# Kernel tuning notes

Measured on AMD Instinct MI355X. Metric: run time of the kernel, lower is better.

## Reference

```python
import jax, jax.numpy as jnp
import numpy as np

N_QUBITS = 13
N_LAYERS = 8
DIM = 2 ** N_QUBITS
CDT = jnp.complex64

_X = jnp.array([[0.0, 1.0], [1.0, 0.0]], dtype=CDT)
_Z = jnp.array([[1.0, 0.0], [0.0, -1.0]], dtype=CDT)
_I2 = jnp.eye(2, dtype=CDT)
_CNOT = jnp.array([[1, 0, 0, 0], [0, 1, 0, 0], [0, 0, 0, 1], [0, 0, 1, 0]], dtype=CDT)


def build_ops():
    """Hardware-efficient ansatz: per layer RX on all qubits, RZ on all qubits, CNOT chain."""
    ops = []
    p = 0
    for _ in range(N_LAYERS):
        for q in range(N_QUBITS):
            ops.append(('RX', (q,), p)); p += 1
        for q in range(N_QUBITS):
            ops.append(('RZ', (q,), p)); p += 1
        for q in range(N_QUBITS - 1):
            ops.append(('CNOT', (q, q + 1), None))
    return ops, p

OPS, N_PARAMS = build_ops()


def _rot(generator, theta):
    # U = cos(theta/2) I - i sin(theta/2) G
    h = theta * 0.5
    return jnp.cos(h).astype(CDT) * _I2 - 1j * jnp.sin(h).astype(CDT) * generator


def _apply_1q(state, U, q):
    st = state.reshape((2,) * N_QUBITS)
    st = jnp.tensordot(U, st, axes=([1], [q]))  # contracted axis moves to front
    return jnp.moveaxis(st, 0, q).reshape(-1)


def _apply_2q(state, U, q0, q1):
    st = state.reshape((2,) * N_QUBITS)
    st = jnp.tensordot(U.reshape(2, 2, 2, 2), st, axes=([2, 3], [q0, q1]))
    return jnp.moveaxis(st, (0, 1), (q0, q1)).reshape(-1)


def _run_circuit(params):
    state = jnp.zeros(DIM, dtype=CDT).at[0].set(1.0)
    for gate, qubits, pidx in OPS:
        if gate == 'RX':
            state = _apply_1q(state, _rot(_X, params[pidx]), qubits[0])
        elif gate == 'RZ':
            state = _apply_1q(state, _rot(_Z, params[pidx]), qubits[0])
        else:  # CNOT
            state = _apply_2q(state, _CNOT, qubits[0], qubits[1])
    return state


def setup_inputs() -> dict:
    key = jax.random.key(0)
    k1, k2 = jax.random.split(key)
    params = jax.random.normal(k1, (N_PARAMS,), dtype=jnp.float32)
    observable = jax.random.normal(k2, (DIM, DIM), dtype=jnp.float32)
    return {"params": params, "observable": observable}


def reference(params, observable) -> jnp.ndarray:
    psi = _run_circuit(params)                      # [2^n] complex64
    obs_psi = observable.astype(CDT) @ psi          # dense observable matvec
    loss = jnp.vdot(psi, obs_psi).real.astype(jnp.float32)  # <psi|O|psi>
    return loss
```

## Files before the change

kernel.cpp:

```cpp
#include <hip/hip_runtime.h>

#define DIM 8192
#define NLAYERS 8
#define SIMT 512
#define QFB 2048
#define QFT 256
#define ROWS_PER_BLOCK 4

typedef float floatx4 __attribute__((ext_vector_type(4)));
typedef float f2 __attribute__((ext_vector_type(2)));

__device__ __forceinline__ int swz(int i) { return i ^ ((i >> 4) & 15); }

__global__ __launch_bounds__(SIMT) void sim_kernel(const float* __restrict__ params,
                                                   float* __restrict__ outR,
                                                   float* __restrict__ outM) {
    __shared__ f2 buf[2][DIM];
    const int t = threadIdx.x;

    f2 a[16];
#pragma unroll
    for (int l = 0; l < 16; ++l) a[l] = (f2){0.f, 0.f};
    if (t == 0) a[0] = (f2){1.f, 0.f};

    int pp = 0;

    for (int layer = 0; layer < NLAYERS; ++layer) {
        const float* __restrict__ prx = params + layer * 26;
        const float* __restrict__ prz = prx + 13;

        float cb[13], sb[13];
#pragma unroll
        for (int p = 0; p < 13; ++p) __sincosf(0.5f * prx[12 - p], &sb[p], &cb[p]);

#pragma unroll
        for (int k = 0; k < 4; ++k) {
            const f2 c2 = {cb[k], cb[k]};
            const f2 sg = {sb[k], -sb[k]};
#pragma unroll
            for (int l0 = 0; l0 < 16; ++l0) {
                if (!(l0 & (1 << k))) {
                    const int l1 = l0 | (1 << k);
                    const f2 a0 = a[l0], a1 = a[l1];
                    a[l0] = c2 * a0 + __builtin_shufflevector(a1, a1, 1, 0) * sg;
                    a[l1] = c2 * a1 + __builtin_shufflevector(a0, a0, 1, 0) * sg;
                }
            }
        }

        {
            f2* __restrict__ B = buf[pp]; pp ^= 1;
#pragma unroll
            for (int l = 0; l < 16; ++l) B[swz((t << 4) | l)] = a[l];
            __syncthreads();
#pragma unroll
            for (int l = 0; l < 16; ++l) a[l] = B[swz((t & 15) | (l << 4) | ((t >> 4) << 8))];
        }

#pragma unroll
        for (int k = 0; k < 4; ++k) {
            const f2 c2 = {cb[4 + k], cb[4 + k]};
            const f2 sg = {sb[4 + k], -sb[4 + k]};
#pragma unroll
            for (int l0 = 0; l0 < 16; ++l0) {
                if (!(l0 & (1 << k))) {
                    const int l1 = l0 | (1 << k);
                    const f2 a0 = a[l0], a1 = a[l1];
                    a[l0] = c2 * a0 + __builtin_shufflevector(a1, a1, 1, 0) * sg;
                    a[l1] = c2 * a1 + __builtin_shufflevector(a0, a0, 1, 0) * sg;
                }
            }
        }

        {
            f2* __restrict__ B = buf[pp]; pp ^= 1;
#pragma unroll
            for (int l = 0; l < 16; ++l) B[swz((t & 15) | (l << 4) | ((t >> 4) << 8))] = a[l];
            __syncthreads();
#pragma unroll
            for (int l = 0; l < 16; ++l)
                a[l] = B[swz(((t >> 1) & 255) | (l << 8) | ((t & 1) << 12))];
        }

#pragma unroll
        for (int k = 0; k < 4; ++k) {
            const f2 c2 = {cb[8 + k], cb[8 + k]};
            const f2 sg = {sb[8 + k], -sb[8 + k]};
#pragma unroll
            for (int l0 = 0; l0 < 16; ++l0) {
                if (!(l0 & (1 << k))) {
                    const int l1 = l0 | (1 << k);
                    const f2 a0 = a[l0], a1 = a[l1];
                    a[l0] = c2 * a0 + __builtin_shufflevector(a1, a1, 1, 0) * sg;
                    a[l1] = c2 * a1 + __builtin_shufflevector(a0, a0, 1, 0) * sg;
                }
            }
        }

        {
            const f2 c2 = {cb[12], cb[12]};
            const f2 sg = {sb[12], -sb[12]};
#pragma unroll
            for (int l = 0; l < 16; ++l) {
                f2 o;
                o.x = __shfl_xor(a[l].x, 1);
                o.y = __shfl_xor(a[l].y, 1);
                a[l] = c2 * a[l] + __builtin_shufflevector(o, o, 1, 0) * sg;
            }
        }

        float hz[13];
#pragma unroll
        for (int p = 0; p < 13; ++p) hz[p] = 0.5f * prz[12 - p];
        float phiT = 0.f;
#pragma unroll
        for (int p = 0; p < 8; ++p) phiT += (((t >> 1) >> p) & 1) ? hz[p] : -hz[p];
        phiT += (t & 1) ? hz[12] : -hz[12];
#pragma unroll
        for (int l = 0; l < 16; ++l) {
            float phi = phiT;
            phi += (l & 1) ? hz[8]  : -hz[8];
            phi += (l & 2) ? hz[9]  : -hz[9];
            phi += (l & 4) ? hz[10] : -hz[10];
            phi += (l & 8) ? hz[11] : -hz[11];
            float sp, cp;
            __sincosf(phi, &sp, &cp);
            a[l] = (f2){a[l].x * cp - a[l].y * sp, a[l].x * sp + a[l].y * cp};
        }

        {
            f2* __restrict__ B = buf[pp]; pp ^= 1;
#pragma unroll
            for (int l = 0; l < 16; ++l)
                B[swz(((t >> 1) & 255) | (l << 8) | ((t & 1) << 12))] = a[l];
            __syncthreads();
#pragma unroll
            for (int l = 0; l < 16; ++l) {
                const int c0 = (t << 4) | l;
                a[l] = B[swz(c0 ^ (c0 >> 1))];
            }
        }
    }

#pragma unroll
    for (int g = 0; g < 4; ++g) {
        const float4 rv = make_float4(a[4*g].x, a[4*g+1].x, a[4*g+2].x, a[4*g+3].x);
        const float4 mv = make_float4(a[4*g].y, a[4*g+1].y, a[4*g+2].y, a[4*g+3].y);
        ((float4*)outR)[(t << 2) + g] = rv;
        ((float4*)outM)[(t << 2) + g] = mv;
    }
}

__global__ __launch_bounds__(QFT) void quad_kernel(const float* __restrict__ O,
                                                   const float* __restrict__ R,
                                                   const float* __restrict__ M,
                                                   float* __restrict__ partials) {
    const int bi = blockIdx.x;
    const int t  = threadIdx.x;
    const float4* __restrict__ R4 = (const float4*)R;
    const float4* __restrict__ M4 = (const float4*)M;

    float acc = 0.f;
#pragma unroll
    for (int rr = 0; rr < ROWS_PER_BLOCK; ++rr) {
        const int i = bi * ROWS_PER_BLOCK + rr;
        const float ri = R[i];
        const float mi = M[i];
        const floatx4* __restrict__ Or = (const floatx4*)(O + (size_t)i * DIM);
#pragma unroll
        for (int it = 0; it < DIM / 4 / QFT; ++it) {
            const int j4 = t + it * QFT;
            const floatx4 o = __builtin_nontemporal_load(&Or[j4]);
            const float4 rj = R4[j4];
            const float4 mj = M4[j4];
            acc = fmaf(o.x, fmaf(ri, rj.x, mi * mj.x), acc);
            acc = fmaf(o.y, fmaf(ri, rj.y, mi * mj.y), acc);
            acc = fmaf(o.z, fmaf(ri, rj.z, mi * mj.z), acc);
            acc = fmaf(o.w, fmaf(ri, rj.w, mi * mj.w), acc);
        }
    }

#pragma unroll
    for (int off = 32; off > 0; off >>= 1) acc += __shfl_down(acc, off);
    __shared__ float wsum[QFT / 64];
    const int lane = t & 63, w = t >> 6;
    if (lane == 0) wsum[w] = acc;
    __syncthreads();
    if (t == 0) {
        float s = 0.f;
#pragma unroll
        for (int k = 0; k < QFT / 64; ++k) s += wsum[k];
        partials[bi] = s;
    }
}

__global__ __launch_bounds__(256) void reduce_kernel(const float* __restrict__ partials,
                                                     float* __restrict__ out) {
    const int t = threadIdx.x;
    float acc = 0.f;
#pragma unroll
    for (int k = 0; k < QFB / 256; ++k) acc += partials[t + k * 256];
#pragma unroll
    for (int off = 32; off > 0; off >>= 1) acc += __shfl_down(acc, off);
    __shared__ float wsum[4];
    const int lane = t & 63, w = t >> 6;
    if (lane == 0) wsum[w] = acc;
    __syncthreads();
    if (t == 0) out[0] = wsum[0] + wsum[1] + wsum[2] + wsum[3];
}

extern "C" void kernel_launch(void* const* d_in, const int* in_sizes, int n_in,
                              void* d_out, int out_size, void* d_ws, size_t ws_size,
                              hipStream_t stream) {
    const float* params = (const float*)d_in[0];
    const float* O      = (const float*)d_in[1];
    float* out = (float*)d_out;

    float* R        = (float*)d_ws;
    float* M        = R + DIM;
    float* partials = M + DIM;

    sim_kernel<<<1, SIMT, 0, stream>>>(params, R, M);
    quad_kernel<<<QFB, QFT, 0, stream>>>(O, R, M, partials);
    reduce_kernel<<<1, 256, 0, stream>>>(partials, out);
}
```

Baseline: 82.15 us.

## Double simulation threads to 1024 with 8 amplitudes each and four-stage exchange

The single-block statevector simulation now uses 1024 threads, each holding 8 amplitudes instead of 16. The qubit passes are regrouped into 3-qubit register stages, which adds one more shared-memory transpose and __syncthreads per layer. The aim is to shorten the serial per-thread dependency chain in the latency-bound single-block kernel, at the cost of more barriers and LDS traffic per layer.

```diff
diff --git a/kernel.cpp b/kernel.cpp
--- a/kernel.cpp
+++ b/kernel.cpp
@@ -2,7 +2,7 @@
 
 #define DIM 8192
 #define NLAYERS 8
-#define SIMT 512
+#define SIMT 1024
 #define QFB 2048
 #define QFT 256
 #define ROWS_PER_BLOCK 4
@@ -18,9 +18,9 @@
     __shared__ f2 buf[2][DIM];
     const int t = threadIdx.x;
 
-    f2 a[16];
-#pragma unroll
-    for (int l = 0; l < 16; ++l) a[l] = (f2){0.f, 0.f};
+    f2 a[8];
+#pragma unroll
+    for (int l = 0; l < 8; ++l) a[l] = (f2){0.f, 0.f};
     if (t == 0) a[0] = (f2){1.f, 0.f};
 
     int pp = 0;
@@ -34,60 +34,88 @@
         for (int p = 0; p < 13; ++p) __sincosf(0.5f * prx[12 - p], &sb[p], &cb[p]);
 
 #pragma unroll
-        for (int k = 0; k < 4; ++k) {
+        for (int k = 0; k < 3; ++k) {
             const f2 c2 = {cb[k], cb[k]};
             const f2 sg = {sb[k], -sb[k]};
 #pragma unroll
-            for (int l0 = 0; l0 < 16; ++l0) {
-                if (!(l0 & (1 << k))) {
-                    const int l1 = l0 | (1 << k);
-                    const f2 a0 = a[l0], a1 = a[l1];
-                    a[l0] = c2 * a0 + __builtin_shufflevector(a1, a1, 1, 0) * sg;
-                    a[l1] = c2 * a1 + __builtin_shufflevector(a0, a0, 1, 0) * sg;
-                }
-            }
-        }
-
-        {
-            f2* __restrict__ B = buf[pp]; pp ^= 1;
-#pragma unroll
-            for (int l = 0; l < 16; ++l) B[swz((t << 4) | l)] = a[l];
-            __syncthreads();
-#pragma unroll
-            for (int l = 0; l < 16; ++l) a[l] = B[swz((t & 15) | (l << 4) | ((t >> 4) << 8))];
-        }
-
-#pragma unroll
-        for (int k = 0; k < 4; ++k) {
-            const f2 c2 = {cb[4 + k], cb[4 + k]};
-            const f2 sg = {sb[4 + k], -sb[4 + k]};
-#pragma unroll
-            for (int l0 = 0; l0 < 16; ++l0) {
-                if (!(l0 & (1 << k))) {
-                    const int l1 = l0 | (1 << k);
-                    const f2 a0 = a[l0], a1 = a[l1];
-                    a[l0] = c2 * a0 + __builtin_shufflevector(a1, a1, 1, 0) * sg;
-                    a[l1] = c2 * a1 + __builtin_shufflevector(a0, a0, 1, 0) * sg;
-                }
-            }
-        }
-
-        {
-            f2* __restrict__ B = buf[pp]; pp ^= 1;
-#pragma unroll
-            for (int l = 0; l < 16; ++l) B[swz((t & 15) | (l << 4) | ((t >> 4) << 8))] = a[l];
-            __syncthreads();
-#pragma unroll
-            for (int l = 0; l < 16; ++l)
-                a[l] = B[swz(((t >> 1) & 255) | (l << 8) | ((t & 1) << 12))];
-        }
-
-#pragma unroll
-        for (int k = 0; k < 4; ++k) {
-            const f2 c2 = {cb[8 + k], cb[8 + k]};
-            const f2 sg = {sb[8 + k], -sb[8 + k]};
-#pragma unroll
-            for (int l0 = 0; l0 < 16; ++l0) {
+            for (int l0 = 0; l0 < 8; ++l0) {
+                if (!(l0 & (1 << k))) {
+                    const int l1 = l0 | (1 << k);
+                    const f2 a0 = a[l0], a1 = a[l1];
+                    a[l0] = c2 * a0 + __builtin_shufflevector(a1, a1, 1, 0) * sg;
+                    a[l1] = c2 * a1 + __builtin_shufflevector(a0, a0, 1, 0) * sg;
+                }
+            }
+        }
+
+        {
+            f2* __restrict__ B = buf[pp]; pp ^= 1;
+#pragma unroll
+            for (int l = 0; l < 8; ++l) B[swz((t << 3) | l)] = a[l];
+            __syncthreads();
+#pragma unroll
+            for (int l = 0; l < 8; ++l)
+                a[l] = B[swz((t & 7) | (l << 3) | ((t >> 3) << 6))];
+        }
+
+#pragma unroll
+        for (int k = 0; k < 3; ++k) {
+            const f2 c2 = {cb[3 + k], cb[3 + k]};
+            const f2 sg = {sb[3 + k], -sb[3 + k]};
+#pragma unroll
+            for (int l0 = 0; l0 < 8; ++l0) {
+                if (!(l0 & (1 << k))) {
+                    const int l1 = l0 | (1 << k);
+                    const f2 a0 = a[l0], a1 = a[l1];
+                    a[l0] = c2 * a0 + __builtin_shufflevector(a1, a1, 1, 0) * sg;
+                    a[l1] = c2 * a1 + __builtin_shufflevector(a0, a0, 1, 0) * sg;
+                }
+            }
+        }
+
+        {
+            f2* __restrict__ B = buf[pp]; pp ^= 1;
+#pragma unroll
+            for (int l = 0; l < 8; ++l)
+                B[swz((t & 7) | (l << 3) | ((t >> 3) << 6))] = a[l];
+            __syncthreads();
+#pragma unroll
+            for (int l = 0; l < 8; ++l)
+                a[l] = B[swz((t & 63) | (l << 6) | ((t >> 6) << 9))];
+        }
+
+#pragma unroll
+        for (int k = 0; k < 3; ++k) {
+            const f2 c2 = {cb[6 + k], cb[6 + k]};
+            const f2 sg = {sb[6 + k], -sb[6 + k]};
+#pragma unroll
+            for (int l0 = 0; l0 < 8; ++l0) {
+                if (!(l0 & (1 << k))) {
+                    const int l1 = l0 | (1 << k);
+                    const f2 a0 = a[l0], a1 = a[l1];
+                    a[l0] = c2 * a0 + __builtin_shufflevector(a1, a1, 1, 0) * sg;
+                    a[l1] = c2 * a1 + __builtin_shufflevector(a0, a0, 1, 0) * sg;
+                }
+            }
+        }
+
+        {
+            f2* __restrict__ B = buf[pp]; pp ^= 1;
+#pragma unroll
+            for (int l = 0; l < 8; ++l)
+                B[swz((t & 63) | (l << 6) | ((t >> 6) << 9))] = a[l];
+            __syncthreads();
+#pragma unroll
+            for (int l = 0; l < 8; ++l)
+                a[l] = B[swz(((t >> 1) & 511) | (l << 9) | ((t & 1) << 12))];
+        }
+
+#pragma unroll
+        for (int k = 0; k < 3; ++k) {
+            const f2 c2 = {cb[9 + k], cb[9 + k]};
+            const f2 sg = {sb[9 + k], -sb[9 + k]};
+#pragma unroll
+            for (int l0 = 0; l0 < 8; ++l0) {
                 if (!(l0 & (1 << k))) {
                     const int l1 = l0 | (1 << k);
                     const f2 a0 = a[l0], a1 = a[l1];
@@ -101,7 +129,7 @@
             const f2 c2 = {cb[12], cb[12]};
             const f2 sg = {sb[12], -sb[12]};
 #pragma unroll
-            for (int l = 0; l < 16; ++l) {
+            for (int l = 0; l < 8; ++l) {
                 f2 o;
                 o.x = __shfl_xor(a[l].x, 1);
                 o.y = __shfl_xor(a[l].y, 1);
@@ -114,15 +142,14 @@
         for (int p = 0; p < 13; ++p) hz[p] = 0.5f * prz[12 - p];
         float phiT = 0.f;
 #pragma unroll
-        for (int p = 0; p < 8; ++p) phiT += (((t >> 1) >> p) & 1) ? hz[p] : -hz[p];
+        for (int p = 0; p < 9; ++p) phiT += (((t >> 1) >> p) & 1) ? hz[p] : -hz[p];
         phiT += (t & 1) ? hz[12] : -hz[12];
 #pragma unroll
-        for (int l = 0; l < 16; ++l) {
+        for (int l = 0; l < 8; ++l) {
             float phi = phiT;
-            phi += (l & 1) ? hz[8]  : -hz[8];
-            phi += (l & 2) ? hz[9]  : -hz[9];
-            phi += (l & 4) ? hz[10] : -hz[10];
-            phi += (l & 8) ? hz[11] : -hz[11];
+            phi += (l & 1) ? hz[9]  : -hz[9];
+            phi += (l & 2) ? hz[10] : -hz[10];
+            phi += (l & 4) ? hz[11] : -hz[11];
             float sp, cp;
             __sincosf(phi, &sp, &cp);
             a[l] = (f2){a[l].x * cp - a[l].y * sp, a[l].x * sp + a[l].y * cp};
@@ -131,23 +158,26 @@
         {
             f2* __restrict__ B = buf[pp]; pp ^= 1;
 #pragma unroll
-            for (int l = 0; l < 16; ++l)
-                B[swz(((t >> 1) & 255) | (l << 8) | ((t & 1) << 12))] = a[l];
-            __syncthreads();
-#pragma unroll
-            for (int l = 0; l < 16; ++l) {
-                const int c0 = (t << 4) | l;
+            for (int l = 0; l < 8; ++l)
+                B[swz(((t >> 1) & 511) | (l << 9) | ((t & 1) << 12))] = a[l];
+            __syncthreads();
+#pragma unroll
+            for (int l = 0; l < 8; ++l) {
+                const int c0 = (t << 3) | l;
                 a[l] = B[swz(c0 ^ (c0 >> 1))];
             }
         }
     }
 
-#pragma unroll
-    for (int g = 0; g < 4; ++g) {
-        const float4 rv = make_float4(a[4*g].x, a[4*g+1].x, a[4*g+2].x, a[4*g+3].x);
-        const float4 mv = make_float4(a[4*g].y, a[4*g+1].y, a[4*g+2].y, a[4*g+3].y);
-        ((float4*)outR)[(t << 2) + g] = rv;
-        ((float4*)outM)[(t << 2) + g] = mv;
+    {
+        const float4 rv0 = make_float4(a[0].x, a[1].x, a[2].x, a[3].x);
+        const float4 rv1 = make_float4(a[4].x, a[5].x, a[6].x, a[7].x);
+        const float4 mv0 = make_float4(a[0].y, a[1].y, a[2].y, a[3].y);
+        const float4 mv1 = make_float4(a[4].y, a[5].y, a[6].y, a[7].y);
+        ((float4*)outR)[2 * t]     = rv0;
+        ((float4*)outR)[2 * t + 1] = rv1;
+        ((float4*)outM)[2 * t]     = mv0;
+        ((float4*)outM)[2 * t + 1] = mv1;
     }
 }
 
```

Result: no change. 80.65 us (-1.8%).
